# Optimization experiments

Measured on AMD Instinct MI355X. Metric: run time of the kernel, lower is better.

Reference implementation:

```python
import jax, jax.numpy as jnp
import numpy as np

D_MODEL, D_K, D_V, H = 1024, 64, 64, 16
B, NQ, NK = 4, 1024, 1024
HID = D_MODEL // 2


def _dwg(x, W1, b1, W2, b2):
    # DynamicWeightGenerator: sigmoid(fc2(relu(fc1(x))))
    h = jax.nn.relu(jnp.einsum('bnd,hd->bnh', x, W1) + b1)
    return jax.nn.sigmoid(jnp.einsum('bnh,dh->bnd', h, W2) + b2)


def setup_inputs() -> dict:
    key = jax.random.key(0)
    ks = jax.random.split(key, 32)
    s = 0.02
    inp = {
        'queries': jax.random.normal(ks[0], (B, NQ, D_MODEL), jnp.float32),
        'keys': jax.random.normal(ks[1], (B, NK, D_MODEL), jnp.float32),
        'values': jax.random.normal(ks[2], (B, NK, D_MODEL), jnp.float32),
        'attention_mask': jax.random.randint(ks[3], (B, 1, NQ, NK), 0, 2) > 0,
        'attention_weights': jax.random.uniform(ks[4], (B, H, NQ, NK), jnp.float32),
        'memory': jax.random.normal(ks[5], (B, NK), jnp.float32),
        # projections (torch Linear convention: y = x @ W.T + b)
        'Wq': jax.random.normal(ks[6], (H * D_K, D_MODEL), jnp.float32) * s,
        'bq': jnp.zeros((H * D_K,), jnp.float32),
        'Wk': jax.random.normal(ks[7], (H * D_K, D_MODEL), jnp.float32) * s,
        'bk': jnp.zeros((H * D_K,), jnp.float32),
        'Wv': jax.random.normal(ks[8], (H * D_V, D_MODEL), jnp.float32) * s,
        'bv': jnp.zeros((H * D_V,), jnp.float32),
        'Wo': jax.random.normal(ks[9], (D_MODEL, H * D_V), jnp.float32) * s,
        'bo': jnp.zeros((D_MODEL,), jnp.float32),
        'Wmm': jax.random.normal(ks[10], (H * D_V, 1), jnp.float32) * s,
        'bmm': jnp.zeros((H * D_V,), jnp.float32),
    }
    for i, tag in enumerate(['q', 'k', 'v']):
        k0, k1 = ks[11 + 2 * i], ks[12 + 2 * i]
        inp[f'W1{tag}'] = jax.random.normal(k0, (HID, D_MODEL), jnp.float32) * s
        inp[f'b1{tag}'] = jnp.zeros((HID,), jnp.float32)
        inp[f'W2{tag}'] = jax.random.normal(k1, (D_MODEL, HID), jnp.float32) * s
        inp[f'b2{tag}'] = jnp.zeros((D_MODEL,), jnp.float32)
    return inp


def reference(queries, keys, values, attention_mask, attention_weights, memory,
              Wq, bq, Wk, bk, Wv, bv, Wo, bo, Wmm, bmm,
              W1q, b1q, W2q, b2q, W1k, b1k, W2k, b2k, W1v, b1v, W2v, b2v):
    b_s, nq = queries.shape[:2]
    nk = keys.shape[1]
    # dynamic elementwise gating of inputs
    q_in = queries * _dwg(queries, W1q, b1q, W2q, b2q)
    k_in = keys * _dwg(keys, W1k, b1k, W2k, b2k)
    v_in = values * _dwg(values, W1v, b1v, W2v, b2v)
    # projections -> (b, h, n, d)
    q = (jnp.einsum('bnd,ed->bne', q_in, Wq) + bq).reshape(b_s, nq, H, D_K).transpose(0, 2, 1, 3)
    k = (jnp.einsum('bnd,ed->bne', k_in, Wk) + bk).reshape(b_s, nk, H, D_K).transpose(0, 2, 1, 3)
    v = (jnp.einsum('bnd,ed->bne', v_in, Wv) + bv).reshape(b_s, nk, H, D_V).transpose(0, 2, 1, 3)
    # per-token memory factor: fc_mm(memory[..., None]) -> (b, h, nk, d_k)
    mm = (memory[..., None] * Wmm[:, 0] + bmm).reshape(b_s, nk, H, D_K).transpose(0, 2, 1, 3)
    att = jnp.einsum('bhqd,bhkd->bhqk', q, k * mm) / np.sqrt(D_K).astype(np.float32)
    att = att * attention_weights                         # custom scaling (slice [:nk] == full)
    att = jnp.where(attention_mask, -jnp.inf, att)        # masked_fill
    att = jax.nn.softmax(att, axis=-1)
    out = jnp.einsum('bhqk,bhkd->bhqd', att, v * mm)      # (b, h, nq, d_v)
    out = out.transpose(0, 2, 1, 3).reshape(b_s, nq, H * D_V)
    return jnp.einsum('bne,de->bnd', out, Wo) + bo
```

## Files before the change

kernel.cpp:

```cpp
#include <hip/hip_runtime.h>
#include <hip/hip_bf16.h>

#define BB    4
#define NN    1024
#define DM    1024
#define HH    16
#define HID   512
#define TT    (BB * NN)

typedef __attribute__((ext_vector_type(8))) short bf16x8;
typedef __attribute__((ext_vector_type(4))) float f32x4;

__device__ __forceinline__ ushort f2bfu(float f) {
    __hip_bfloat16 h = __float2bfloat16(f);
    return __builtin_bit_cast(ushort, h);
}

__device__ __forceinline__ float bfu2f(ushort u) {
    __hip_bfloat16 h = __builtin_bit_cast(__hip_bfloat16, u);
    return __bfloat162float(h);
}

__device__ __forceinline__ f32x4 mfma16(bf16x8 a, bf16x8 b, f32x4 c) {
    return __builtin_amdgcn_mfma_f32_16x16x32_bf16(a, b, c, 0, 0, 0);
}

__device__ __forceinline__ void gll16(const void* g, void* l) {
    __builtin_amdgcn_global_load_lds(
        (const __attribute__((address_space(1))) unsigned int*)g,
        (__attribute__((address_space(3))) unsigned int*)l, 16, 0, 0);
}

__global__ void detect_mask_kernel(const uint4* __restrict__ m,
                                   int n16, int* __restrict__ flags) {
    int stride = blockDim.x * gridDim.x;
    unsigned hi = 0, lo = 0;
    for (int i = blockIdx.x * blockDim.x + threadIdx.x; i < n16; i += stride) {
        uint4 v = m[i];
        unsigned o = v.x | v.y | v.z | v.w;
        lo |= o & 0xFFu;
        hi |= o & 0xFFFFFF00u;
    }
    if (hi) atomicOr(&flags[0], 1);
    if (lo) atomicOr(&flags[1], 1);
}

template <int NS>
struct CvtArgs { const float* s[NS]; ushort* d[NS]; };

template <int NS>
__global__ __launch_bounds__(256) void cvt_multi(CvtArgs<NS> a, int n4) {
    int total = n4 * NS;
    int stride = blockDim.x * gridDim.x;
    for (int i = blockIdx.x * blockDim.x + threadIdx.x; i < total; i += stride) {
        const float* sp = a.s[0];
        ushort* dp = a.d[0];
        #pragma unroll
        for (int k = 1; k < NS; ++k) {
            bool ge = i >= k * n4;
            sp = ge ? a.s[k] : sp;
            dp = ge ? a.d[k] : dp;
        }
        int j = i % n4;
        float4 v = ((const float4*)sp)[j];
        uint2 o;
        o.x = (unsigned)f2bfu(v.x) | ((unsigned)f2bfu(v.y) << 16);
        o.y = (unsigned)f2bfu(v.z) | ((unsigned)f2bfu(v.w) << 16);
        ((uint2*)dp)[j] = o;
    }
}

struct GB {
    const ushort* A[3]; const ushort* W[3];
    const float* bias[3]; void* C[3]; const ushort* X[3];
};

template <int EP, int NF>
__global__ __launch_bounds__(256) void gemm_bf16(
    GB gb, int M, int N, int K,
    const float* __restrict__ mem, const float* __restrict__ Wmm,
    const float* __restrict__ bmm)
{
    __shared__ __align__(16) ushort As[2][128 * 64];
    __shared__ __align__(16) ushort Bs[2][NF * 32 * 64];
    const int z = blockIdx.z;
    const ushort* A = gb.A[z];
    const ushort* W = gb.W[z];
    const float* bias = gb.bias[z];
    void* Cout = gb.C[z];
    const ushort* X = gb.X[z];

    const int tid = threadIdx.x;
    const int lane = tid & 63, w = tid >> 6;
    const int lc = lane & 15, lg = lane >> 4;
    const int m0 = blockIdx.x * 128, n0 = blockIdx.y * (NF * 32);
    const int wm = (w >> 1) * 64, wn = (w & 1) * (NF * 16);
    const int srow = lane >> 3, scol = 8 * ((lane & 7) ^ srow);
    const int swl = (lc & 7) << 3;

    f32x4 acc[4][NF];
    #pragma unroll
    for (int i = 0; i < 4; ++i)
        #pragma unroll
        for (int j = 0; j < NF; ++j)
            acc[i][j] = (f32x4){0.f, 0.f, 0.f, 0.f};

    auto stage = [&](int buf, int k0) {
        #pragma unroll
        for (int ci = 0; ci < 4; ++ci) {
            int c = w + ci * 4;
            gll16(&A[(size_t)(m0 + c * 8 + srow) * K + k0 + scol], &As[buf][c * 512]);
            if (c < NF * 4)
                gll16(&W[(size_t)(n0 + c * 8 + srow) * K + k0 + scol], &Bs[buf][c * 512]);
        }
    };

    stage(0, 0);
    stage(1, 64);
    const int nt = K / 64;

    for (int t = 0; t < nt; ++t) {
        const int cur = t & 1;
        if (t < nt - 1) {
            if constexpr (NF == 4) asm volatile("s_waitcnt vmcnt(8)" ::: "memory");
            else                   asm volatile("s_waitcnt vmcnt(6)" ::: "memory");
        } else {
            asm volatile("s_waitcnt vmcnt(0)" ::: "memory");
        }
        __builtin_amdgcn_sched_barrier(0);
        __builtin_amdgcn_s_barrier();

        bf16x8 af[4][2], bfr[NF][2];
        #pragma unroll
        for (int mi = 0; mi < 4; ++mi) {
            int row = wm + mi * 16 + lc;
            af[mi][0] = *(const bf16x8*)&As[cur][row * 64 + ((lg * 8) ^ swl)];
            af[mi][1] = *(const bf16x8*)&As[cur][row * 64 + ((32 + lg * 8) ^ swl)];
        }
        #pragma unroll
        for (int nj = 0; nj < NF; ++nj) {
            int row = wn + nj * 16 + lc;
            bfr[nj][0] = *(const bf16x8*)&Bs[cur][row * 64 + ((lg * 8) ^ swl)];
            bfr[nj][1] = *(const bf16x8*)&Bs[cur][row * 64 + ((32 + lg * 8) ^ swl)];
        }
        asm volatile("s_waitcnt lgkmcnt(0)" ::: "memory");
        __builtin_amdgcn_sched_barrier(0);
        __builtin_amdgcn_s_barrier();

        if (t + 2 < nt) stage(cur, (t + 2) * 64);

        #pragma unroll
        for (int mi = 0; mi < 4; ++mi)
            #pragma unroll
            for (int nj = 0; nj < NF; ++nj) {
                acc[mi][nj] = mfma16(af[mi][0], bfr[nj][0], acc[mi][nj]);
                acc[mi][nj] = mfma16(af[mi][1], bfr[nj][1], acc[mi][nj]);
            }
    }

    #pragma unroll
    for (int nj = 0; nj < NF; ++nj) {
        int e = n0 + wn + nj * 16 + lc;
        float bv = bias[e];
        float wmv = 0.f, bmv = 0.f;
        if (EP == 7) { wmv = Wmm[e]; bmv = bmm[e]; }
        #pragma unroll
        for (int mi = 0; mi < 4; ++mi) {
            int mbase = m0 + wm + mi * 16 + lg * 4;
            if (EP == 7 && z == 2) {
                ushort u[4];
                #pragma unroll
                for (int r = 0; r < 4; ++r) {
                    float v = (acc[mi][nj][r] + bv) * (mem[mbase + r] * wmv + bmv);
                    u[r] = f2bfu(v);
                }
                int bb = mbase >> 10, n = mbase & 1023;
                size_t off = ((size_t)(bb * HH + (e >> 6)) * 64 + (e & 63)) * NN + n;
                uint2 pk;
                pk.x = (unsigned)u[0] | ((unsigned)u[1] << 16);
                pk.y = (unsigned)u[2] | ((unsigned)u[3] << 16);
                *(uint2*)&((ushort*)Cout)[off] = pk;
            } else {
                #pragma unroll
                for (int r = 0; r < 4; ++r) {
                    int m = mbase + r;
                    float v = acc[mi][nj][r] + bv;
                    if (EP == 1) v = fmaxf(v, 0.f);
                    if (EP == 2) v = bfu2f(X[(size_t)m * N + e]) * (1.f / (1.f + __expf(-v)));
                    if (EP == 7) {
                        if (z == 0) v = v * 0.125f;
                        else        v = v * (mem[m] * wmv + bmv);
                    }
                    size_t off = (size_t)m * N + e;
                    if (EP == 4) ((float*)Cout)[off] = v;
                    else         ((ushort*)Cout)[off] = f2bfu(v);
                }
            }
        }
    }
}

__global__ __launch_bounds__(256) void attn_mfma(
    const ushort* __restrict__ qp, const ushort* __restrict__ kp,
    const ushort* __restrict__ vt, const float* __restrict__ aw,
    const void* __restrict__ maskp, const int* __restrict__ mflags,
    ushort* __restrict__ ob)
{
    __shared__ __align__(16) ushort Ks[2][64 * 64];
    __shared__ __align__(16) ushort Vs[2][64 * 64];
    __shared__ __align__(16) ushort Ps[64 * 64];
    const int tid = threadIdx.x, lane = tid & 63, w = tid >> 6;
    const int lc = lane & 15, lg = lane >> 4;
    const int bid = blockIdx.x;
    const int swz = (bid & 7) * 128 + (bid >> 3);
    const int qt = swz & 15, bh = swz >> 4;
    const int b = bh >> 4, h = bh & 15;
    const int q0 = qt * 64, wq = w * 16;
    const int mode = mflags[0] ? (mflags[1] ? 1 : 2) : 0;
    const int srow = lane >> 3, scol = 8 * ((lane & 7) ^ srow);
    const int swl = (lc & 7) << 3;

    const ushort* qrow = &qp[(size_t)(b * NN + q0 + wq + lc) * DM + h * 64];
    bf16x8 bq0 = *(const bf16x8*)&qrow[lg * 8];
    bf16x8 bq1 = *(const bf16x8*)&qrow[32 + lg * 8];

    f32x4 oacc[4];
    #pragma unroll
    for (int i = 0; i < 4; ++i) oacc[i] = (f32x4){0.f, 0.f, 0.f, 0.f};
    float psum = 0.f;
    const int q = q0 + wq + lc;
    const float* awrow = aw + ((size_t)bh * NN + q) * NN;
    const size_t mrowo = ((size_t)b * NN + q) * NN;

    float4 awA[4], awB[4];
    uint4 mk4A[4], mk4B[4];
    unsigned mk1A[4], mk1B[4];

    #pragma unroll
    for (int ci = 0; ci < 2; ++ci) {
        int c = w + ci * 4;
        gll16(&kp[(size_t)(b * NN + c * 8 + srow) * DM + h * 64 + scol], &Ks[0][c * 512]);
        gll16(&vt[((size_t)bh * 64 + c * 8 + srow) * NN + 0 + scol], &Vs[0][c * 512]);
    }
    #pragma unroll
    for (int mi = 0; mi < 4; ++mi)
        awA[mi] = *(const float4*)&awrow[mi * 16 + lg * 4];
    if (mode == 1) {
        #pragma unroll
        for (int mi = 0; mi < 4; ++mi)
            mk1A[mi] = *(const unsigned*)&((const unsigned char*)maskp)[mrowo + mi * 16 + lg * 4];
    } else {
        #pragma unroll
        for (int mi = 0; mi < 4; ++mi)
            mk4A[mi] = *(const uint4*)((const char*)maskp + 4 * (mrowo + mi * 16 + lg * 4));
    }
    asm volatile("s_waitcnt vmcnt(0)" ::: "memory");
    __builtin_amdgcn_sched_barrier(0);
    __builtin_amdgcn_s_barrier();

#define ATTN_BODY(T, AWC, MK4C, MK1C, AWN, MK4N, MK1N)                          \
    {                                                                           \
        const int cur = (T) & 1;                                                \
        if ((T) < 15) {                                                         \
            const int kn = ((T) + 1) * 64;                                      \
            _Pragma("unroll")                                                   \
            for (int ci = 0; ci < 2; ++ci) {                                    \
                int c = w + ci * 4;                                             \
                gll16(&kp[(size_t)(b * NN + kn + c * 8 + srow) * DM + h * 64 + scol], \
                      &Ks[cur ^ 1][c * 512]);                                   \
                gll16(&vt[((size_t)bh * 64 + c * 8 + srow) * NN + kn + scol],   \
                      &Vs[cur ^ 1][c * 512]);                                   \
            }                                                                   \
            __builtin_amdgcn_sched_barrier(0);                                  \
            _Pragma("unroll")                                                   \
            for (int mi = 0; mi < 4; ++mi)                                      \
                AWN[mi] = *(const float4*)&awrow[kn + mi * 16 + lg * 4];        \
            if (mode == 1) {                                                    \
                _Pragma("unroll")                                               \
                for (int mi = 0; mi < 4; ++mi)                                  \
                    MK1N[mi] = *(const unsigned*)&((const unsigned char*)maskp) \
                                   [mrowo + kn + mi * 16 + lg * 4];             \
            } else {                                                            \
                _Pragma("unroll")                                               \
                for (int mi = 0; mi < 4; ++mi)                                  \
                    MK4N[mi] = *(const uint4*)((const char*)maskp +             \
                                   4 * (mrowo + kn + mi * 16 + lg * 4));        \
            }                                                                   \
            __builtin_amdgcn_sched_barrier(0);                                  \
        }                                                                       \
                                                               \
        f32x4 sacc[4];                                                          \
        __builtin_amdgcn_s_setprio(1);                                          \
        _Pragma("unroll")                                                       \
        for (int mi = 0; mi < 4; ++mi) {                                        \
            int krow = mi * 16 + lc;                                            \
            bf16x8 a0 = *(const bf16x8*)&Ks[cur][krow * 64 + ((lg * 8) ^ swl)]; \
            bf16x8 a1 = *(const bf16x8*)&Ks[cur][krow * 64 + ((32 + lg * 8) ^ swl)]; \
            f32x4 s = (f32x4){0.f, 0.f, 0.f, 0.f};                              \
            s = mfma16(a0, bq0, s);                                             \
            s = mfma16(a1, bq1, s);                                             \
            sacc[mi] = s;                                                       \
        }                                                                       \
        __builtin_amdgcn_s_setprio(0);                                          \
                                 \
        _Pragma("unroll")                                                       \
        for (int mi = 0; mi < 4; ++mi) {                                        \
            unsigned mk[4];                                                     \
            if (mode == 1) {                                                    \
                mk[0] = MK1C[mi] & 0xffu;         mk[1] = (MK1C[mi] >> 8) & 0xffu;  \
                mk[2] = (MK1C[mi] >> 16) & 0xffu; mk[3] = (MK1C[mi] >> 24) & 0xffu; \
            } else if (mode == 0) {                                             \
                mk[0] = MK4C[mi].x; mk[1] = MK4C[mi].y;                         \
                mk[2] = MK4C[mi].z; mk[3] = MK4C[mi].w;                         \
            } else {                                                            \
                mk[0] = MK4C[mi].x != 0; mk[1] = MK4C[mi].y != 0;               \
                mk[2] = MK4C[mi].z != 0; mk[3] = MK4C[mi].w != 0;               \
            }                                                                   \
            const float aww[4] = {AWC[mi].x, AWC[mi].y, AWC[mi].z, AWC[mi].w};  \
            float pv[4];                                                        \
            _Pragma("unroll")                                                   \
            for (int r = 0; r < 4; ++r) {                                       \
                float sv = sacc[mi][r] * aww[r];                                \
                pv[r] = mk[r] ? 0.f : __expf(sv);                               \
                psum += pv[r];                                                  \
            }                                                                   \
            uint2 pk;                                                           \
            pk.x = (unsigned)f2bfu(pv[0]) | ((unsigned)f2bfu(pv[1]) << 16);     \
            pk.y = (unsigned)f2bfu(pv[2]) | ((unsigned)f2bfu(pv[3]) << 16);     \
            *(uint2*)&Ps[(wq + lc) * 64 + ((mi * 16 + lg * 4) ^ swl)] = pk;     \
        }                                                                       \
                                                                        \
        __builtin_amdgcn_s_setprio(1);                                          \
        _Pragma("unroll")                                                       \
        for (int kk = 0; kk < 2; ++kk) {                                        \
            bf16x8 pa = *(const bf16x8*)&Ps[(wq + lc) * 64 + ((kk * 32 + lg * 8) ^ swl)]; \
            _Pragma("unroll")                                                   \
            for (int nj = 0; nj < 4; ++nj) {                                    \
                bf16x8 vb = *(const bf16x8*)&Vs[cur][(nj * 16 + lc) * 64 + ((kk * 32 + lg * 8) ^ swl)]; \
                oacc[nj] = mfma16(pa, vb, oacc[nj]);                            \
            }                                                                   \
        }                                                                       \
        __builtin_amdgcn_s_setprio(0);                                          \
        if ((T) < 15) {                                                         \
            asm volatile("s_waitcnt vmcnt(8)" ::: "memory");                    \
            __builtin_amdgcn_sched_barrier(0);                                  \
            __builtin_amdgcn_s_barrier();                                       \
        }                                                                       \
    }

    for (int tt = 0; tt < 8; ++tt) {
        const int t0 = tt * 2, t1 = tt * 2 + 1;
        ATTN_BODY(t0, awA, mk4A, mk1A, awB, mk4B, mk1B);
        ATTN_BODY(t1, awB, mk4B, mk1B, awA, mk4A, mk1A);
    }
#undef ATTN_BODY

    psum += __shfl_xor(psum, 16);
    psum += __shfl_xor(psum, 32);
    float inv = 1.0f / psum;
    float invr[4];
    #pragma unroll
    for (int r = 0; r < 4; ++r)
        invr[r] = __shfl(inv, (lane & 48) | (lg * 4 + r));

    #pragma unroll
    for (int nj = 0; nj < 4; ++nj)
        #pragma unroll
        for (int r = 0; r < 4; ++r) {
            int qq = q0 + wq + lg * 4 + r;
            float v = oacc[nj][r] * invr[r];
            ob[(size_t)(b * NN + qq) * DM + h * 64 + nj * 16 + lc] = f2bfu(v);
        }
}

extern "C" void kernel_launch(void* const* d_in, const int* in_sizes, int n_in,
                              void* d_out, int out_size, void* d_ws, size_t ws_size,
                              hipStream_t stream) {
    const float* xin_f[3] = {(const float*)d_in[0], (const float*)d_in[1], (const float*)d_in[2]};
    const void*  maskp   = d_in[3];
    const float* aw      = (const float*)d_in[4];
    const float* memv    = (const float*)d_in[5];
    const float* Wp_f[3] = {(const float*)d_in[6], (const float*)d_in[8], (const float*)d_in[10]};
    const float* bp[3]   = {(const float*)d_in[7], (const float*)d_in[9], (const float*)d_in[11]};
    const float* Wo_f  = (const float*)d_in[12];  const float* bo  = (const float*)d_in[13];
    const float* Wmm = (const float*)d_in[14];    const float* bmm = (const float*)d_in[15];
    const float* W1f[3] = {(const float*)d_in[16], (const float*)d_in[20], (const float*)d_in[24]};
    const float* b1a[3] = {(const float*)d_in[17], (const float*)d_in[21], (const float*)d_in[25]};
    const float* W2f[3] = {(const float*)d_in[18], (const float*)d_in[22], (const float*)d_in[26]};
    const float* b2a[3] = {(const float*)d_in[19], (const float*)d_in[23], (const float*)d_in[27]};

    char* p = (char*)d_ws;
    auto alloc = [&](size_t bytes) { char* r = p; p += (bytes + 255) & ~(size_t)255; return r; };
    int*    mflags = (int*)alloc(256);
    ushort* xbf[3]; for (int t = 0; t < 3; ++t) xbf[t] = (ushort*)alloc((size_t)TT * DM * 2);
    ushort* Wpb[3]; for (int t = 0; t < 3; ++t) Wpb[t] = (ushort*)alloc((size_t)DM * DM * 2);
    ushort* Wob  = (ushort*)alloc((size_t)DM * DM * 2);
    ushort* W1b[3]; for (int t = 0; t < 3; ++t) W1b[t] = (ushort*)alloc((size_t)HID * DM * 2);
    ushort* W2b[3]; for (int t = 0; t < 3; ++t) W2b[t] = (ushort*)alloc((size_t)DM * HID * 2);
    ushort* hbuf[3]; for (int t = 0; t < 3; ++t) hbuf[t] = (ushort*)alloc((size_t)TT * HID * 2);
    ushort* xg[3];  for (int t = 0; t < 3; ++t) xg[t] = (ushort*)alloc((size_t)TT * DM * 2);
    ushort* qpb  = (ushort*)alloc((size_t)TT * DM * 2);
    ushort* ksb  = (ushort*)alloc((size_t)TT * DM * 2);
    ushort* vtb  = (ushort*)alloc((size_t)TT * DM * 2);
    ushort* obuf = (ushort*)alloc((size_t)TT * DM * 2);

    hipMemsetAsync(mflags, 0, 8, stream);
    detect_mask_kernel<<<256, 256, 0, stream>>>((const uint4*)maskp,
                                                BB * NN * NN / 16, mflags);

    {
        CvtArgs<3> a;
        for (int t = 0; t < 3; ++t) { a.s[t] = xin_f[t]; a.d[t] = xbf[t]; }
        cvt_multi<3><<<2048, 256, 0, stream>>>(a, TT * DM / 4);
    }
    {
        CvtArgs<4> a;
        a.s[0] = Wp_f[0]; a.d[0] = Wpb[0];
        a.s[1] = Wp_f[1]; a.d[1] = Wpb[1];
        a.s[2] = Wp_f[2]; a.d[2] = Wpb[2];
        a.s[3] = Wo_f;    a.d[3] = Wob;
        cvt_multi<4><<<2048, 256, 0, stream>>>(a, DM * DM / 4);
    }
    {
        CvtArgs<6> a;
        for (int t = 0; t < 3; ++t) { a.s[t] = W1f[t]; a.d[t] = W1b[t]; }
        for (int t = 0; t < 3; ++t) { a.s[3 + t] = W2f[t]; a.d[3 + t] = W2b[t]; }
        cvt_multi<6><<<2048, 256, 0, stream>>>(a, HID * DM / 4);
    }

    const dim3 blk(256);
    GB g1 = {}, g2 = {}, g3 = {}, g4 = {};
    for (int t = 0; t < 3; ++t) {
        g1.A[t] = xbf[t];  g1.W[t] = W1b[t]; g1.bias[t] = b1a[t]; g1.C[t] = hbuf[t];
        g2.A[t] = hbuf[t]; g2.W[t] = W2b[t]; g2.bias[t] = b2a[t]; g2.C[t] = xg[t]; g2.X[t] = xbf[t];
        g3.A[t] = xg[t];   g3.W[t] = Wpb[t]; g3.bias[t] = bp[t];
    }
    g3.C[0] = qpb; g3.C[1] = ksb; g3.C[2] = vtb;
    g4.A[0] = obuf; g4.W[0] = Wob; g4.bias[0] = bo; g4.C[0] = d_out;

    gemm_bf16<1, 2><<<dim3(TT / 128, HID / 64, 3), blk, 0, stream>>>(g1, TT, HID, DM, nullptr, nullptr, nullptr);
    gemm_bf16<2, 4><<<dim3(TT / 128, DM / 128, 3), blk, 0, stream>>>(g2, TT, DM, HID, nullptr, nullptr, nullptr);
    gemm_bf16<7, 4><<<dim3(TT / 128, DM / 128, 3), blk, 0, stream>>>(g3, TT, DM, DM, memv, Wmm, bmm);

    attn_mfma<<<dim3(NN / 16 * (BB * HH) / 4), blk, 0, stream>>>(qpb, ksb, vtb, aw,
                                                                 maskp, mflags, obuf);

    gemm_bf16<4, 2><<<dim3(TT / 128, DM / 64, 1), blk, 0, stream>>>(g4, TT, DM, DM, nullptr, nullptr, nullptr);
}
```

Measured before the change: 269.7 us.

## Merge conversion kernels, shrink GEMM N-tiles, and tighten attention wait count

Folds the three fp32-to-bf16 conversion launches into one kernel that picks its segment from cumulative bounds, removing two launches. The gating-fc2 and projection GEMMs move from 128-wide to 64-wide N tiles, doubling their grid size for better occupancy at the cost of less operand reuse. The attention loop now waits for all outstanding global loads (vmcnt 0) instead of leaving 8 in flight, which may reduce prefetch overlap. The attention grid size is written as a literal with the same value as before.

```diff
diff --git a/kernel.cpp b/kernel.cpp
--- a/kernel.cpp
+++ b/kernel.cpp
@@ -45,23 +45,23 @@
     if (lo) atomicOr(&flags[1], 1);
 }
 
-template <int NS>
-struct CvtArgs { const float* s[NS]; ushort* d[NS]; };
-
-template <int NS>
-__global__ __launch_bounds__(256) void cvt_multi(CvtArgs<NS> a, int n4) {
-    int total = n4 * NS;
+#define NSEG 13
+struct CvtAll { const float* s[NSEG]; ushort* d[NSEG]; int bound[NSEG]; };
+
+__global__ __launch_bounds__(256) void cvt_all(CvtAll a, int total) {
     int stride = blockDim.x * gridDim.x;
     for (int i = blockIdx.x * blockDim.x + threadIdx.x; i < total; i += stride) {
         const float* sp = a.s[0];
         ushort* dp = a.d[0];
-        #pragma unroll
-        for (int k = 1; k < NS; ++k) {
-            bool ge = i >= k * n4;
+        int base = 0;
+        #pragma unroll
+        for (int k = 1; k < NSEG; ++k) {
+            bool ge = i >= a.bound[k - 1];
             sp = ge ? a.s[k] : sp;
             dp = ge ? a.d[k] : dp;
-        }
-        int j = i % n4;
+            base = ge ? a.bound[k - 1] : base;
+        }
+        int j = i - base;
         float4 v = ((const float4*)sp)[j];
         uint2 o;
         o.x = (unsigned)f2bfu(v.x) | ((unsigned)f2bfu(v.y) << 16);
@@ -342,7 +342,7 @@
         }                                                                       \
         __builtin_amdgcn_s_setprio(0);                                          \
         if ((T) < 15) {                                                         \
-            asm volatile("s_waitcnt vmcnt(8)" ::: "memory");                    \
+            asm volatile("s_waitcnt vmcnt(0)" ::: "memory");                    \
             __builtin_amdgcn_sched_barrier(0);                                  \
             __builtin_amdgcn_s_barrier();                                       \
         }                                                                       \
@@ -409,23 +409,18 @@
                                                 BB * NN * NN / 16, mflags);
 
     {
-        CvtArgs<3> a;
-        for (int t = 0; t < 3; ++t) { a.s[t] = xin_f[t]; a.d[t] = xbf[t]; }
-        cvt_multi<3><<<2048, 256, 0, stream>>>(a, TT * DM / 4);
-    }
-    {
-        CvtArgs<4> a;
-        a.s[0] = Wp_f[0]; a.d[0] = Wpb[0];
-        a.s[1] = Wp_f[1]; a.d[1] = Wpb[1];
-        a.s[2] = Wp_f[2]; a.d[2] = Wpb[2];
-        a.s[3] = Wo_f;    a.d[3] = Wob;
-        cvt_multi<4><<<2048, 256, 0, stream>>>(a, DM * DM / 4);
-    }
-    {
-        CvtArgs<6> a;
-        for (int t = 0; t < 3; ++t) { a.s[t] = W1f[t]; a.d[t] = W1b[t]; }
-        for (int t = 0; t < 3; ++t) { a.s[3 + t] = W2f[t]; a.d[3 + t] = W2b[t]; }
-        cvt_multi<6><<<2048, 256, 0, stream>>>(a, HID * DM / 4);
+        CvtAll a;
+        const int S_IN = TT * DM / 4, S_W = DM * DM / 4, S_H = HID * DM / 4;
+        int idx = 0, cum = 0;
+        auto seg = [&](const float* s, ushort* d, int n) {
+            a.s[idx] = s; a.d[idx] = d; cum += n; a.bound[idx] = cum; ++idx;
+        };
+        for (int t = 0; t < 3; ++t) seg(xin_f[t], xbf[t], S_IN);
+        for (int t = 0; t < 3; ++t) seg(Wp_f[t], Wpb[t], S_W);
+        seg(Wo_f, Wob, S_W);
+        for (int t = 0; t < 3; ++t) seg(W1f[t], W1b[t], S_H);
+        for (int t = 0; t < 3; ++t) seg(W2f[t], W2b[t], S_H);
+        cvt_all<<<2048, 256, 0, stream>>>(a, cum);
     }
 
     const dim3 blk(256);
@@ -439,11 +434,11 @@
     g4.A[0] = obuf; g4.W[0] = Wob; g4.bias[0] = bo; g4.C[0] = d_out;
 
     gemm_bf16<1, 2><<<dim3(TT / 128, HID / 64, 3), blk, 0, stream>>>(g1, TT, HID, DM, nullptr, nullptr, nullptr);
-    gemm_bf16<2, 4><<<dim3(TT / 128, DM / 128, 3), blk, 0, stream>>>(g2, TT, DM, HID, nullptr, nullptr, nullptr);
-    gemm_bf16<7, 4><<<dim3(TT / 128, DM / 128, 3), blk, 0, stream>>>(g3, TT, DM, DM, memv, Wmm, bmm);
-
-    attn_mfma<<<dim3(NN / 16 * (BB * HH) / 4), blk, 0, stream>>>(qpb, ksb, vtb, aw,
-                                                                 maskp, mflags, obuf);
+    gemm_bf16<2, 2><<<dim3(TT / 128, DM / 64, 3), blk, 0, stream>>>(g2, TT, DM, HID, nullptr, nullptr, nullptr);
+    gemm_bf16<7, 2><<<dim3(TT / 128, DM / 64, 3), blk, 0, stream>>>(g3, TT, DM, DM, memv, Wmm, bmm);
+
+    attn_mfma<<<dim3(1024), blk, 0, stream>>>(qpb, ksb, vtb, aw,
+                                              maskp, mflags, obuf);
 
     gemm_bf16<4, 2><<<dim3(TT / 128, DM / 64, 1), blk, 0, stream>>>(g4, TT, DM, DM, nullptr, nullptr, nullptr);
 }
```

Measured after the change: 260.9 us. -3.3%, faster.
